# Optimization experiments

Hardware: AMD Instinct MI355X
Metric: run time of the kernel (lower is better)

The kernel has to match this reference:

```python
import jax, jax.numpy as jnp
import numpy as np

N_HEAD = 16


def setup_inputs() -> dict:
    key = jax.random.key(0)
    k0, k1, k2, k3 = jax.random.split(key, 4)
    b, n, d = 4, 2048, 1024
    scale = d ** -0.5
    return {
        "x": jax.random.normal(k0, (b, n, d), jnp.float32),
        "Wk": jax.random.normal(k1, (d, d), jnp.float32) * scale,
        "Wq": jax.random.normal(k2, (d, d), jnp.float32) * scale,
        "Wv": jax.random.normal(k3, (d, d), jnp.float32) * scale,
    }


def reference(x, Wk, Wq, Wv):
    b, n, d = x.shape
    hd = d // N_HEAD
    # Linear layers: y = x @ W^T (torch nn.Linear convention), no bias.
    keys = (x @ Wk.T).reshape(b, n, N_HEAD, hd).transpose(0, 2, 1, 3)     # (b,h,n,hd)
    queries = (x @ Wq.T).reshape(b, n, N_HEAD, hd).transpose(0, 2, 1, 3)  # (b,h,n,hd)
    values = (x @ Wv.T).reshape(b, n, N_HEAD, hd).transpose(0, 2, 1, 3)   # computed but UNUSED, as in source
    del values
    # Source does: attn_scores = keys @ queries.transpose(-1,-2)
    # i.e. scores[b,h,i,j] = k_i . q_j ; softmax over j (query axis); no 1/sqrt(d) scaling.
    attn_scores = jnp.einsum("bhid,bhjd->bhij", keys, queries)
    weights = jax.nn.softmax(attn_scores, axis=-1)
    # Source does: weight_scores @ keys (keys, NOT values)
    weighted = jnp.einsum("bhij,bhjd->bhid", weights, keys)  # (b,h,n,hd)
    # Source reshapes (b,h,n,hd) directly to (b,n,h*hd) WITHOUT transposing back.
    return weighted.reshape(b, n, N_HEAD * hd)
```

## Files before the change

kernel.cpp:

```cpp
#include <hip/hip_runtime.h>
#include <cstdint>
#include <cstddef>

#define NTOK 2048
#define DMODEL 1024
#define HD 64
#define MROWS 8192

using f16x8  = __attribute__((ext_vector_type(8))) _Float16;
using f16x4  = __attribute__((ext_vector_type(4))) _Float16;
using f16x2  = __attribute__((ext_vector_type(2))) _Float16;
using f32x4  = __attribute__((ext_vector_type(4))) float;
using f32x16 = __attribute__((ext_vector_type(16))) float;
using u32x4  = __attribute__((ext_vector_type(4))) unsigned int;

#define Z16 {0.f,0.f,0.f,0.f,0.f,0.f,0.f,0.f,0.f,0.f,0.f,0.f,0.f,0.f,0.f,0.f}

extern "C" __device__ _Float16 __ocml_exp2_f16(_Float16);

__device__ __forceinline__ void plswap(unsigned &a, unsigned &b) {
  auto r = __builtin_amdgcn_permlane32_swap(a, b, false, false);
  a = r[0]; b = r[1];
}
__device__ __forceinline__ float fexp2(float x) {
  return __builtin_amdgcn_exp2f(x);
}
__device__ __forceinline__ float fmax3(float a, float b, float c) {
  return fmaxf(fmaxf(a, b), c);
}
__device__ __forceinline__ unsigned pk2h(_Float16 lo, _Float16 hi) {
  return (unsigned)__builtin_bit_cast(unsigned short, lo) |
         ((unsigned)__builtin_bit_cast(unsigned short, hi) << 16);
}

__global__ __launch_bounds__(256) void cvt_f32_f16(const float* __restrict__ in,
                                                   _Float16* __restrict__ out,
                                                   int n4, float scale) {
  int idx = blockIdx.x * 256 + threadIdx.x;
  if (idx < n4) {
    float4 v = reinterpret_cast<const float4*>(in)[idx];
    f16x4 o;
    o.x = (_Float16)(v.x * scale); o.y = (_Float16)(v.y * scale);
    o.z = (_Float16)(v.z * scale); o.w = (_Float16)(v.w * scale);
    reinterpret_cast<f16x4*>(out)[idx] = o;
  }
}

__global__ __launch_bounds__(256) void cvt_w(const float* __restrict__ Wk,
                                             const float* __restrict__ Wq,
                                             _Float16* __restrict__ Wkb,
                                             _Float16* __restrict__ Wqb) {
  const int idx = blockIdx.x * 256 + threadIdx.x;
  const float* in = blockIdx.y ? Wq : Wk;
  _Float16* out = blockIdx.y ? Wqb : Wkb;
  const float scale = blockIdx.y ? 1.4426950408889634f : 1.0f;
  float4 v = reinterpret_cast<const float4*>(in)[idx];
  f16x4 o;
  o.x = (_Float16)(v.x * scale); o.y = (_Float16)(v.y * scale);
  o.z = (_Float16)(v.z * scale); o.w = (_Float16)(v.w * scale);
  reinterpret_cast<f16x4*>(out)[idx] = o;
}

#define GLDS16(g, l) __builtin_amdgcn_global_load_lds(                      \
    (const __attribute__((address_space(1))) void*)(g),                     \
    (__attribute__((address_space(3))) void*)(l), 16, 0, 0)

__global__ __launch_bounds__(256) void gemm_pack_f16(
    const _Float16* __restrict__ X,
    const _Float16* __restrict__ Wk,
    const _Float16* __restrict__ Wq,
    _Float16* __restrict__ Kp,
    _Float16* __restrict__ Qp) {
  const bool isQ = blockIdx.z != 0;
  const _Float16* __restrict__ W = isQ ? Wq : Wk;

  __shared__ _Float16 arena[17408];
  _Float16* As = arena;
  _Float16* Bs = arena + 8192;

  const int tid = threadIdx.x;
  const int lane = tid & 63;
  const int w = tid >> 6;
  const int m0 = blockIdx.x * 128;
  const int o0 = blockIdx.y * 128;

  const int srow = w * 32 + (lane >> 2);
  const int scol = (lane & 3) * 8;
  const _Float16* xsrc = X + (size_t)(m0 + srow) * DMODEL + scol;
  const _Float16* wsrc = W + (size_t)(o0 + srow) * DMODEL + scol;

  const int wr = w >> 1, wc = w & 1;
  const int arow = lane & 15, kg = lane >> 4;
  const int l31 = lane & 31, hi8 = (lane >> 5) * 8;

  f32x4 zero = {0.f, 0.f, 0.f, 0.f};
  f32x4 acc[4][4];
#pragma unroll
  for (int mi = 0; mi < 4; ++mi)
#pragma unroll
    for (int ni = 0; ni < 4; ++ni) acc[mi][ni] = zero;

  GLDS16(xsrc,               &As[(w * 32) * 32]);
  GLDS16(xsrc + 16 * DMODEL, &As[(w * 32 + 16) * 32]);
  GLDS16(wsrc,               &Bs[(w * 32) * 32]);
  GLDS16(wsrc + 16 * DMODEL, &Bs[(w * 32 + 16) * 32]);

  for (int kt = 0; kt < 32; ++kt) {
    __syncthreads();
    if (kt + 1 < 32) {
      const int ko = (kt + 1) * 32;
      const int bo = ((kt + 1) & 1) * 4096;
      GLDS16(xsrc + ko,               &As[bo + (w * 32) * 32]);
      GLDS16(xsrc + ko + 16 * DMODEL, &As[bo + (w * 32 + 16) * 32]);
      GLDS16(wsrc + ko,               &Bs[bo + (w * 32) * 32]);
      GLDS16(wsrc + ko + 16 * DMODEL, &Bs[bo + (w * 32 + 16) * 32]);
    }
    const int bo = (kt & 1) * 4096;
    f16x8 af[4], bfr[4];
#pragma unroll
    for (int mi = 0; mi < 4; ++mi)
      af[mi] = *reinterpret_cast<const f16x8*>(
          &As[bo + (wr * 64 + mi * 16 + arow) * 32 + kg * 8]);
#pragma unroll
    for (int ni = 0; ni < 4; ++ni)
      bfr[ni] = *reinterpret_cast<const f16x8*>(
          &Bs[bo + (wc * 64 + ni * 16 + arow) * 32 + kg * 8]);
#pragma unroll
    for (int mi = 0; mi < 4; ++mi)
#pragma unroll
      for (int ni = 0; ni < 4; ++ni)
        acc[mi][ni] = __builtin_amdgcn_mfma_f32_16x16x32_f16(
            af[mi], bfr[ni], acc[mi][ni], 0, 0, 0);
  }

  __syncthreads();
  _Float16* T = arena;
#pragma unroll
  for (int mi = 0; mi < 4; ++mi)
#pragma unroll
    for (int ni = 0; ni < 4; ++ni)
#pragma unroll
      for (int r = 0; r < 4; ++r)
        T[(wr * 64 + mi * 16 + kg * 4 + r) * 136 + wc * 64 + ni * 16 + arow] =
            (_Float16)acc[mi][ni][r];
  __syncthreads();

  const int b = m0 >> 11;
  _Float16* RowDst = isQ ? Qp : Kp;
#pragma unroll
  for (int k = 0; k < 8; ++k) {
    const int c = w * 8 + k;
    const int hl = c >> 4, rtl = (c >> 2) & 3, ks = c & 3;
    f16x8 v = *reinterpret_cast<const f16x8*>(
        &T[(rtl * 32 + l31) * 136 + hl * 64 + ks * 16 + hi8]);
    const int bh = b * 16 + (o0 >> 6) + hl;
    const int rt = ((m0 & 2047) >> 5) + rtl;
    const size_t ch = ((size_t)(bh * 64 + rt) * 4 + ks) * 512 + (size_t)lane * 8;
    *reinterpret_cast<f16x8*>(&RowDst[ch]) = v;
  }
}

__global__ __launch_bounds__(256) void pack_kt(
    const _Float16* __restrict__ Kp,
    _Float16* __restrict__ KTp) {
  const int blk = blockIdx.x;
  const int bh = blk >> 5;
  const int t64 = blk & 31;
  const int tid = threadIdx.x;
  const int l = tid & 63;

  __shared__ _Float16 t[64][72];
#pragma unroll
  for (int pass = 0; pass < 2; ++pass) {
    const int idx = pass * 4 + (tid >> 6);
    const int rs = idx >> 2, ks = idx & 3;
    f16x8 v = *reinterpret_cast<const f16x8*>(
        &Kp[((size_t)(bh * 64 + t64 * 2 + rs) * 4 + ks) * 512 + (size_t)l * 8]);
    *reinterpret_cast<f16x8*>(&t[rs * 32 + (l & 31)][ks * 16 + (l >> 5) * 8]) = v;
  }
  __syncthreads();
#pragma unroll
  for (int pass = 0; pass < 2; ++pass) {
    const int idx = pass * 4 + (tid >> 6);
    const int ds = idx >> 2, ks = idx & 3;
    const int row0 = ks * 16 + (l >> 5) * 8;
    const int col = ds * 32 + (l & 31);
    f16x8 v;
#pragma unroll
    for (int e = 0; e < 8; ++e) v[e] = t[row0 + e][col];
    const size_t ch = (((size_t)(bh * 32 + t64) * 2 + ds) * 4 + ks) * 512 + (size_t)l * 8;
    *reinterpret_cast<f16x8*>(&KTp[ch]) = v;
  }
}

__global__ __launch_bounds__(256, 3) void attn_mfma(
    const _Float16* __restrict__ Kp,
    const _Float16* __restrict__ Qp,
    const _Float16* __restrict__ KTp,
    float* __restrict__ out) {
  const int bid = blockIdx.x;
  const int myid = (bid & 7) * 256 + (bid >> 3);
  const int bh = myid >> 5;
  const int itile = myid & 31;
  const int tid = threadIdx.x, lane = tid & 63, w = tid >> 6;
  const int l31 = lane & 31;
  const int hi = lane >> 5;
  const int i_sub = w & 1;
  const int jh = w >> 1;
  const int i0 = itile * 64 + i_sub * 32;

  const _Float16* kpp  = Kp  + (size_t)bh * 131072 + lane * 8;
  const _Float16* qpp  = Qp  + (size_t)bh * 131072 + lane * 8;
  const _Float16* ktpp = KTp + (size_t)bh * 131072 + lane * 8;

  __shared__ float scl[4][32];
  __shared__ float mM[2][2][32];
  __shared__ float lsM[2][2][32];
  __shared__ float obuf[2][32][64];

  f16x8 kbf[4];
#pragma unroll
  for (int ks = 0; ks < 4; ++ks)
    kbf[ks] = *reinterpret_cast<const f16x8*>(
        kpp + ((size_t)(i0 >> 5) * 4 + ks) * 512);

  const f32x16 z16v = Z16;
  f32x16 o0 = z16v, o1 = z16v;
  float mreg = -1e30f, ls = 0.f;
  const f16x2 one2 = {(_Float16)1.f, (_Float16)1.f};

  const _Float16* qP  = qpp  + (size_t)jh * 65536;
  const _Float16* ktP = ktpp + (size_t)jh * 65536;

#define ATT_TILE(QO, KTO)                                                     \
  {                                                                           \
    f16x8 q[4];                                                               \
    _Pragma("unroll")                                                         \
    for (int ks = 0; ks < 4; ++ks)                                            \
      q[ks] = *reinterpret_cast<const f16x8*>(qP + (QO) + ks * 512);          \
    f32x16 s = z16v;                                                          \
    __builtin_amdgcn_s_setprio(1);                                            \
    _Pragma("unroll")                                                         \
    for (int ks = 0; ks < 4; ++ks)                                            \
      s = __builtin_amdgcn_mfma_f32_32x32x16_f16(q[ks], kbf[ks], s, 0, 0, 0); \
    __builtin_amdgcn_s_setprio(0);                                            \
    f16x8 kt0[2], kt1[2];                                                     \
    kt0[0] = *reinterpret_cast<const f16x8*>(ktP + (KTO));                    \
    kt0[1] = *reinterpret_cast<const f16x8*>(ktP + (KTO) + 512);              \
    kt1[0] = *reinterpret_cast<const f16x8*>(ktP + (KTO) + 2048);             \
    kt1[1] = *reinterpret_cast<const f16x8*>(ktP + (KTO) + 2560);             \
    float t0 = fmax3(s[0], s[1], s[2]);                                       \
    float t1 = fmax3(s[3], s[4], s[5]);                                       \
    float t2 = fmax3(s[6], s[7], s[8]);                                       \
    float t3 = fmax3(s[9], s[10], s[11]);                                     \
    float t4 = fmax3(s[12], s[13], s[14]);                                    \
    float pm = fmaxf(fmax3(t0, t1, t2), fmax3(t3, t4, s[15]));                \
    pm = fmaxf(pm, __shfl_xor(pm, 32));                                       \
    if (!__all(pm <= mreg + 8.0f)) {                                          \
      const float mn = fmaxf(mreg, pm);                                       \
      const float sc = fexp2(mreg - mn);                                      \
      ls *= sc;                                                               \
      mreg = mn;                                                              \
      scl[w][l31] = sc;                                                       \
      _Pragma("unroll")                                                       \
      for (int r = 0; r < 16; ++r) {                                          \
        const int il = (r & 3) + 8 * (r >> 2) + 4 * hi;                       \
        const float scr = scl[w][il];                                         \
        o0[r] *= scr; o1[r] *= scr;                                           \
      }                                                                       \
    }                                                                         \
      \
    _Float16 pe[16];                                                          \
    _Pragma("unroll")                                                         \
    for (int r = 0; r < 16; ++r)                                              \
      pe[r] = __ocml_exp2_f16((_Float16)(s[r] - mreg));                       \
    unsigned a0 = pk2h(pe[0], pe[1]),   b0 = pk2h(pe[4], pe[5]);              \
    unsigned a1 = pk2h(pe[2], pe[3]),   b1 = pk2h(pe[6], pe[7]);              \
    unsigned a2 = pk2h(pe[8], pe[9]),   b2 = pk2h(pe[12], pe[13]);            \
    unsigned a3 = pk2h(pe[10], pe[11]), b3 = pk2h(pe[14], pe[15]);            \
              \
    {                                                                         \
      float sA = __builtin_amdgcn_fdot2(__builtin_bit_cast(f16x2, a0), one2,  \
                                        0.f, false);                          \
      sA = __builtin_amdgcn_fdot2(__builtin_bit_cast(f16x2, a1), one2, sA, false);\
      sA = __builtin_amdgcn_fdot2(__builtin_bit_cast(f16x2, a2), one2, sA, false);\
      sA = __builtin_amdgcn_fdot2(__builtin_bit_cast(f16x2, a3), one2, sA, false);\
      float sB = __builtin_amdgcn_fdot2(__builtin_bit_cast(f16x2, b0), one2,  \
                                        0.f, false);                          \
      sB = __builtin_amdgcn_fdot2(__builtin_bit_cast(f16x2, b1), one2, sB, false);\
      sB = __builtin_amdgcn_fdot2(__builtin_bit_cast(f16x2, b2), one2, sB, false);\
      sB = __builtin_amdgcn_fdot2(__builtin_bit_cast(f16x2, b3), one2, sB, false);\
      ls += sA + sB;                                                          \
    }                                                                         \
    f16x8 pfr[2];                                                             \
    {                                                                         \
      plswap(a0, b0); plswap(a1, b1);                                         \
      u32x4 t; t[0] = a0; t[1] = a1; t[2] = b0; t[3] = b1;                    \
      pfr[0] = __builtin_bit_cast(f16x8, t);                                  \
      plswap(a2, b2); plswap(a3, b3);                                         \
      t[0] = a2; t[1] = a3; t[2] = b2; t[3] = b3;                             \
      pfr[1] = __builtin_bit_cast(f16x8, t);                                  \
    }                                                                         \
    __builtin_amdgcn_s_setprio(1);                                            \
    _Pragma("unroll")                                                         \
    for (int kk = 0; kk < 2; ++kk) {                                          \
      o0 = __builtin_amdgcn_mfma_f32_32x32x16_f16(pfr[kk], kt0[kk], o0, 0,0,0);\
      o1 = __builtin_amdgcn_mfma_f32_32x32x16_f16(pfr[kk], kt1[kk], o1, 0,0,0);\
    }                                                                         \
    __builtin_amdgcn_s_setprio(0);                                            \
  }

  for (int it = 0; it < 16; ++it) {
    ATT_TILE(0, 0)
    ATT_TILE(2048, 1024)
    qP += 4096;
    ktP += 4096;
  }
#undef ATT_TILE

  mM[i_sub][jh][l31]  = mreg;
  lsM[i_sub][jh][l31] = ls + __shfl_xor(ls, 32);
  __syncthreads();

  if (jh == 1) {
#pragma unroll
    for (int r = 0; r < 16; ++r) {
      const int il = (r & 3) + 8 * (r >> 2) + 4 * hi;
      const float mS = fmaxf(mM[i_sub][0][il], mM[i_sub][1][il]);
      const float f = fexp2(mM[i_sub][1][il] - mS);
      obuf[i_sub][r][lane]      = o0[r] * f;
      obuf[i_sub][r + 16][lane] = o1[r] * f;
    }
  }
  __syncthreads();
  if (jh == 0) {
#pragma unroll
    for (int r = 0; r < 16; ++r) {
      const int il = (r & 3) + 8 * (r >> 2) + 4 * hi;
      const float mA = mM[i_sub][0][il], mB = mM[i_sub][1][il];
      const float mS = fmaxf(mA, mB);
      const float fA = fexp2(mA - mS);
      const float fB = fexp2(mB - mS);
      const float lsS = lsM[i_sub][0][il] * fA + lsM[i_sub][1][il] * fB;
      const float inv = 1.0f / lsS;
      const size_t rowb = ((size_t)bh * NTOK + i0 + il) * HD;
      out[rowb + l31]      = (o0[r] * fA + obuf[i_sub][r][lane]) * inv;
      out[rowb + 32 + l31] = (o1[r] * fA + obuf[i_sub][r + 16][lane]) * inv;
    }
  }
}

extern "C" void kernel_launch(void* const* d_in, const int* in_sizes, int n_in,
                              void* d_out, int out_size, void* d_ws, size_t ws_size,
                              hipStream_t stream) {
  const float* x  = (const float*)d_in[0];
  const float* Wk = (const float*)d_in[1];
  const float* Wq = (const float*)d_in[2];
  float* out = (float*)d_out;

  _Float16* xb  = (_Float16*)d_ws;
  _Float16* KTp = xb;
  _Float16* Wkb = xb + (size_t)8388608;
  _Float16* Wqb = Wkb + (size_t)1048576;
  _Float16* Kp  = Wqb + (size_t)1048576;
  _Float16* Qp  = Kp + (size_t)8388608;

  cvt_f32_f16<<<8192, 256, 0, stream>>>(x, xb, 2097152, 1.0f);
  cvt_w<<<dim3(1024, 2), 256, 0, stream>>>(Wk, Wq, Wkb, Wqb);

  dim3 ggrid(MROWS / 128, DMODEL / 128, 2);
  gemm_pack_f16<<<ggrid, 256, 0, stream>>>(xb, Wkb, Wqb, Kp, Qp);

  pack_kt<<<2048, 256, 0, stream>>>(Kp, KTp);

  attn_mfma<<<2048, 256, 0, stream>>>(Kp, Qp, KTp, out);
}
```

Measured before the change: 177.5 us.

## Fuse conversions, emit K-transpose from GEMM, prefetch attention tiles, use f32 exp

After: 165.7 us. -6.7%, faster.

```diff
diff --git a/kernel.cpp b/kernel.cpp
--- a/kernel.cpp
+++ b/kernel.cpp
@@ -9,15 +9,15 @@
 
 using f16x8  = __attribute__((ext_vector_type(8))) _Float16;
 using f16x4  = __attribute__((ext_vector_type(4))) _Float16;
-using f16x2  = __attribute__((ext_vector_type(2))) _Float16;
 using f32x4  = __attribute__((ext_vector_type(4))) float;
 using f32x16 = __attribute__((ext_vector_type(16))) float;
 using u32x4  = __attribute__((ext_vector_type(4))) unsigned int;
 
 #define Z16 {0.f,0.f,0.f,0.f,0.f,0.f,0.f,0.f,0.f,0.f,0.f,0.f,0.f,0.f,0.f,0.f}
 
-extern "C" __device__ _Float16 __ocml_exp2_f16(_Float16);
-
+__device__ __forceinline__ unsigned pkf16(float a, float b) {
+  return __builtin_bit_cast(unsigned, __builtin_amdgcn_cvt_pkrtz(a, b));
+}
 __device__ __forceinline__ void plswap(unsigned &a, unsigned &b) {
   auto r = __builtin_amdgcn_permlane32_swap(a, b, false, false);
   a = r[0]; b = r[1];
@@ -28,32 +28,28 @@
 __device__ __forceinline__ float fmax3(float a, float b, float c) {
   return fmaxf(fmaxf(a, b), c);
 }
-__device__ __forceinline__ unsigned pk2h(_Float16 lo, _Float16 hi) {
-  return (unsigned)__builtin_bit_cast(unsigned short, lo) |
-         ((unsigned)__builtin_bit_cast(unsigned short, hi) << 16);
-}
-
-__global__ __launch_bounds__(256) void cvt_f32_f16(const float* __restrict__ in,
-                                                   _Float16* __restrict__ out,
-                                                   int n4, float scale) {
-  int idx = blockIdx.x * 256 + threadIdx.x;
-  if (idx < n4) {
-    float4 v = reinterpret_cast<const float4*>(in)[idx];
-    f16x4 o;
-    o.x = (_Float16)(v.x * scale); o.y = (_Float16)(v.y * scale);
-    o.z = (_Float16)(v.z * scale); o.w = (_Float16)(v.w * scale);
-    reinterpret_cast<f16x4*>(out)[idx] = o;
-  }
-}
-
-__global__ __launch_bounds__(256) void cvt_w(const float* __restrict__ Wk,
-                                             const float* __restrict__ Wq,
-                                             _Float16* __restrict__ Wkb,
-                                             _Float16* __restrict__ Wqb) {
-  const int idx = blockIdx.x * 256 + threadIdx.x;
-  const float* in = blockIdx.y ? Wq : Wk;
-  _Float16* out = blockIdx.y ? Wqb : Wkb;
-  const float scale = blockIdx.y ? 1.4426950408889634f : 1.0f;
+
+__global__ __launch_bounds__(256) void cvt_all(const float* __restrict__ x,
+                                               const float* __restrict__ Wk,
+                                               const float* __restrict__ Wq,
+                                               _Float16* __restrict__ xb,
+                                               _Float16* __restrict__ Wkb,
+                                               _Float16* __restrict__ Wqb) {
+  const int blk = blockIdx.x;
+  const float* in;
+  _Float16* out;
+  float scale;
+  int idx;
+  if (blk < 8192) {
+    in = x; out = xb; scale = 1.0f;
+    idx = blk * 256 + threadIdx.x;
+  } else if (blk < 9216) {
+    in = Wk; out = Wkb; scale = 1.0f;
+    idx = (blk - 8192) * 256 + threadIdx.x;
+  } else {
+    in = Wq; out = Wqb; scale = 1.4426950408889634f;
+    idx = (blk - 9216) * 256 + threadIdx.x;
+  }
   float4 v = reinterpret_cast<const float4*>(in)[idx];
   f16x4 o;
   o.x = (_Float16)(v.x * scale); o.y = (_Float16)(v.y * scale);
@@ -70,7 +66,9 @@
     const _Float16* __restrict__ Wk,
     const _Float16* __restrict__ Wq,
     _Float16* __restrict__ Kp,
-    _Float16* __restrict__ Qp) {
+    _Float16* __restrict__ Qp,
+    _Float16* __restrict__ KTp,
+    int emitKT) {
   const bool isQ = blockIdx.z != 0;
   const _Float16* __restrict__ W = isQ ? Wq : Wk;
 
@@ -157,6 +155,24 @@
     const int rt = ((m0 & 2047) >> 5) + rtl;
     const size_t ch = ((size_t)(bh * 64 + rt) * 4 + ks) * 512 + (size_t)lane * 8;
     *reinterpret_cast<f16x8*>(&RowDst[ch]) = v;
+  }
+
+  if (!isQ && emitKT) {
+#pragma unroll
+    for (int k = 0; k < 8; ++k) {
+      const int c = w * 8 + k;
+      const int hl = c >> 4, jtl = (c >> 3) & 1, ds = (c >> 2) & 1, ks = c & 3;
+      const int row0 = jtl * 64 + ks * 16 + (lane >> 5) * 8;
+      const int col = hl * 64 + ds * 32 + l31;
+      f16x8 v;
+#pragma unroll
+      for (int e = 0; e < 8; ++e) v[e] = T[(row0 + e) * 136 + col];
+      const int bh = b * 16 + (o0 >> 6) + hl;
+      const int jt = ((m0 & 2047) >> 6) + jtl;
+      const size_t ch =
+          (((size_t)(bh * 32 + jt) * 2 + ds) * 4 + ks) * 512 + (size_t)lane * 8;
+      *reinterpret_cast<f16x8*>(&KTp[ch]) = v;
+    }
   }
 }
 
@@ -227,28 +243,33 @@
   const f32x16 z16v = Z16;
   f32x16 o0 = z16v, o1 = z16v;
   float mreg = -1e30f, ls = 0.f;
-  const f16x2 one2 = {(_Float16)1.f, (_Float16)1.f};
-
-  const _Float16* qP  = qpp  + (size_t)jh * 65536;
-  const _Float16* ktP = ktpp + (size_t)jh * 65536;
-
-#define ATT_TILE(QO, KTO)                                                     \
+
+  const int jt0 = jh * 32;
+
+  f16x8 qA[4], qB[4], ktA0[2], ktA1[2], ktB0[2], ktB1[2];
+
+#define LOADT(QD, KT0, KT1, JT)                                               \
   {                                                                           \
-    f16x8 q[4];                                                               \
     _Pragma("unroll")                                                         \
     for (int ks = 0; ks < 4; ++ks)                                            \
-      q[ks] = *reinterpret_cast<const f16x8*>(qP + (QO) + ks * 512);          \
+      QD[ks] = *reinterpret_cast<const f16x8*>(                               \
+          qpp + ((size_t)(JT) * 4 + ks) * 512);                               \
+    const size_t base =                                                       \
+        ((size_t)((JT) >> 1) * 8 + (size_t)((JT) & 1) * 2) * 512;             \
+    KT0[0] = *reinterpret_cast<const f16x8*>(ktpp + base);                    \
+    KT0[1] = *reinterpret_cast<const f16x8*>(ktpp + base + 512);              \
+    KT1[0] = *reinterpret_cast<const f16x8*>(ktpp + base + 2048);             \
+    KT1[1] = *reinterpret_cast<const f16x8*>(ktpp + base + 2560);             \
+  }
+
+#define PROC(Q, KT0, KT1)                                                     \
+  {                                                                           \
     f32x16 s = z16v;                                                          \
     __builtin_amdgcn_s_setprio(1);                                            \
     _Pragma("unroll")                                                         \
     for (int ks = 0; ks < 4; ++ks)                                            \
-      s = __builtin_amdgcn_mfma_f32_32x32x16_f16(q[ks], kbf[ks], s, 0, 0, 0); \
+      s = __builtin_amdgcn_mfma_f32_32x32x16_f16(Q[ks], kbf[ks], s, 0, 0, 0); \
     __builtin_amdgcn_s_setprio(0);                                            \
-    f16x8 kt0[2], kt1[2];                                                     \
-    kt0[0] = *reinterpret_cast<const f16x8*>(ktP + (KTO));                    \
-    kt0[1] = *reinterpret_cast<const f16x8*>(ktP + (KTO) + 512);              \
-    kt1[0] = *reinterpret_cast<const f16x8*>(ktP + (KTO) + 2048);             \
-    kt1[1] = *reinterpret_cast<const f16x8*>(ktP + (KTO) + 2560);             \
     float t0 = fmax3(s[0], s[1], s[2]);                                       \
     float t1 = fmax3(s[3], s[4], s[5]);                                       \
     float t2 = fmax3(s[6], s[7], s[8]);                                       \
@@ -269,34 +290,24 @@
         o0[r] *= scr; o1[r] *= scr;                                           \
       }                                                                       \
     }                                                                         \
-      \
-    _Float16 pe[16];                                                          \
     _Pragma("unroll")                                                         \
-    for (int r = 0; r < 16; ++r)                                              \
-      pe[r] = __ocml_exp2_f16((_Float16)(s[r] - mreg));                       \
-    unsigned a0 = pk2h(pe[0], pe[1]),   b0 = pk2h(pe[4], pe[5]);              \
-    unsigned a1 = pk2h(pe[2], pe[3]),   b1 = pk2h(pe[6], pe[7]);              \
-    unsigned a2 = pk2h(pe[8], pe[9]),   b2 = pk2h(pe[12], pe[13]);            \
-    unsigned a3 = pk2h(pe[10], pe[11]), b3 = pk2h(pe[14], pe[15]);            \
-              \
+    for (int r = 0; r < 16; ++r) s[r] = fexp2(s[r] - mreg);                   \
     {                                                                         \
-      float sA = __builtin_amdgcn_fdot2(__builtin_bit_cast(f16x2, a0), one2,  \
-                                        0.f, false);                          \
-      sA = __builtin_amdgcn_fdot2(__builtin_bit_cast(f16x2, a1), one2, sA, false);\
-      sA = __builtin_amdgcn_fdot2(__builtin_bit_cast(f16x2, a2), one2, sA, false);\
-      sA = __builtin_amdgcn_fdot2(__builtin_bit_cast(f16x2, a3), one2, sA, false);\
-      float sB = __builtin_amdgcn_fdot2(__builtin_bit_cast(f16x2, b0), one2,  \
-                                        0.f, false);                          \
-      sB = __builtin_amdgcn_fdot2(__builtin_bit_cast(f16x2, b1), one2, sB, false);\
-      sB = __builtin_amdgcn_fdot2(__builtin_bit_cast(f16x2, b2), one2, sB, false);\
-      sB = __builtin_amdgcn_fdot2(__builtin_bit_cast(f16x2, b3), one2, sB, false);\
-      ls += sA + sB;                                                          \
+      float l0 = (s[0] + s[4]) + (s[8] + s[12]);                              \
+      float l1 = (s[1] + s[5]) + (s[9] + s[13]);                              \
+      float l2 = (s[2] + s[6]) + (s[10] + s[14]);                             \
+      float l3 = (s[3] + s[7]) + (s[11] + s[15]);                             \
+      ls += (l0 + l1) + (l2 + l3);                                            \
     }                                                                         \
     f16x8 pfr[2];                                                             \
     {                                                                         \
+      unsigned a0 = pkf16(s[0], s[1]),  b0 = pkf16(s[4], s[5]);               \
+      unsigned a1 = pkf16(s[2], s[3]),  b1 = pkf16(s[6], s[7]);               \
       plswap(a0, b0); plswap(a1, b1);                                         \
       u32x4 t; t[0] = a0; t[1] = a1; t[2] = b0; t[3] = b1;                    \
       pfr[0] = __builtin_bit_cast(f16x8, t);                                  \
+      unsigned a2 = pkf16(s[8], s[9]),   b2 = pkf16(s[12], s[13]);            \
+      unsigned a3 = pkf16(s[10], s[11]), b3 = pkf16(s[14], s[15]);            \
       plswap(a2, b2); plswap(a3, b3);                                         \
       t[0] = a2; t[1] = a3; t[2] = b2; t[3] = b3;                             \
       pfr[1] = __builtin_bit_cast(f16x8, t);                                  \
@@ -304,19 +315,22 @@
     __builtin_amdgcn_s_setprio(1);                                            \
     _Pragma("unroll")                                                         \
     for (int kk = 0; kk < 2; ++kk) {                                          \
-      o0 = __builtin_amdgcn_mfma_f32_32x32x16_f16(pfr[kk], kt0[kk], o0, 0,0,0);\
-      o1 = __builtin_amdgcn_mfma_f32_32x32x16_f16(pfr[kk], kt1[kk], o1, 0,0,0);\
+      o0 = __builtin_amdgcn_mfma_f32_32x32x16_f16(pfr[kk], KT0[kk], o0, 0,0,0);\
+      o1 = __builtin_amdgcn_mfma_f32_32x32x16_f16(pfr[kk], KT1[kk], o1, 0,0,0);\
     }                                                                         \
     __builtin_amdgcn_s_setprio(0);                                            \
   }
 
+  LOADT(qA, ktA0, ktA1, jt0)
   for (int it = 0; it < 16; ++it) {
-    ATT_TILE(0, 0)
-    ATT_TILE(2048, 1024)
-    qP += 4096;
-    ktP += 4096;
-  }
-#undef ATT_TILE
+    const int jtA = jt0 + it * 2;
+    LOADT(qB, ktB0, ktB1, jtA + 1)
+    PROC(qA, ktA0, ktA1)
+    if (it < 15) LOADT(qA, ktA0, ktA1, jtA + 2)
+    PROC(qB, ktB0, ktB1)
+  }
+#undef LOADT
+#undef PROC
 
   mM[i_sub][jh][l31]  = mreg;
   lsM[i_sub][jh][l31] = ls + __shfl_xor(ls, 32);
@@ -359,19 +373,20 @@
   float* out = (float*)d_out;
 
   _Float16* xb  = (_Float16*)d_ws;
-  _Float16* KTp = xb;
   _Float16* Wkb = xb + (size_t)8388608;
   _Float16* Wqb = Wkb + (size_t)1048576;
   _Float16* Kp  = Wqb + (size_t)1048576;
   _Float16* Qp  = Kp + (size_t)8388608;
-
-  cvt_f32_f16<<<8192, 256, 0, stream>>>(x, xb, 2097152, 1.0f);
-  cvt_w<<<dim3(1024, 2), 256, 0, stream>>>(Wk, Wq, Wkb, Wqb);
+  const bool fuseKT = ws_size >= (size_t)71303168;
+  _Float16* KTp = fuseKT ? (Qp + (size_t)8388608) : xb;
+
+  cvt_all<<<10240, 256, 0, stream>>>(x, Wk, Wq, xb, Wkb, Wqb);
 
   dim3 ggrid(MROWS / 128, DMODEL / 128, 2);
-  gemm_pack_f16<<<ggrid, 256, 0, stream>>>(xb, Wkb, Wqb, Kp, Qp);
-
-  pack_kt<<<2048, 256, 0, stream>>>(Kp, KTp);
+  gemm_pack_f16<<<ggrid, 256, 0, stream>>>(xb, Wkb, Wqb, Kp, Qp, KTp,
+                                           fuseKT ? 1 : 0);
+
+  if (!fuseKT) pack_kt<<<2048, 256, 0, stream>>>(Kp, KTp);
 
   attn_mfma<<<2048, 256, 0, stream>>>(Kp, Qp, KTp, out);
 }
```
